# Kernel tuning notes

Measured on AMD Instinct MI355X. Metric: run time of the kernel, lower is better.

The kernel has to match this reference:

```python
import jax, jax.numpy as jnp
import numpy as np

N = 100000   # nodes
E = 1600000  # edges
D = 128      # input_dim == hidden_dim
G = 64       # graphs in batch
EPS = 1e-5


def setup_inputs() -> dict:
    key = jax.random.key(0)
    ks = jax.random.split(key, 16)
    s = 1.0 / np.sqrt(D)
    inp = {
        "x": jax.random.normal(ks[0], (N, D), jnp.float32),
        "edge_index": jax.random.randint(ks[1], (2, E), 0, N, jnp.int64),
        "batch": jnp.sort(jax.random.randint(ks[2], (N,), 0, G, jnp.int64)),
        # 4 blocks x 2 SAGEConv layers = 8 convs, all DxD
        "Wl": jax.random.normal(ks[3], (8, D, D), jnp.float32) * s,
        "bl": jnp.zeros((8, D), jnp.float32),
        "Wr": jax.random.normal(ks[4], (8, D, D), jnp.float32) * s,
        "gamma": jnp.ones((4, D), jnp.float32),
        "beta": jnp.zeros((4, D), jnp.float32),
        # classifier: 2D -> D -> D//2 -> 1
        "W1": jax.random.normal(ks[5], (2 * D, D), jnp.float32) / np.sqrt(2 * D),
        "b1": jnp.zeros((D,), jnp.float32),
        "W2": jax.random.normal(ks[6], (D, D // 2), jnp.float32) * s,
        "b2": jnp.zeros((D // 2,), jnp.float32),
        "W3": jax.random.normal(ks[7], (D // 2, 1), jnp.float32) / np.sqrt(D // 2),
        "b3": jnp.zeros((1,), jnp.float32),
    }
    return inp


def _sage_conv(h, src, dst, inv_deg, W_l, b_l, W_r):
    # mean-aggregate neighbor features (messages flow src -> dst)
    agg = jax.ops.segment_sum(h[src], dst, num_segments=N) * inv_deg
    return agg @ W_l + b_l + h @ W_r


def _forward(x, edge_index, batch, Wl, bl, Wr, gamma, beta, W1, b1, W2, b2, W3, b3):
    src, dst = edge_index[0], edge_index[1]
    deg = jax.ops.segment_sum(jnp.ones((E,), x.dtype), dst, num_segments=N)
    inv_deg = (1.0 / jnp.maximum(deg, 1.0))[:, None]  # [N,1]

    h = x
    for blk in range(4):
        # GraphSAGE(in, hid, num_layers=2): conv -> relu -> conv
        h = _sage_conv(h, src, dst, inv_deg, Wl[2 * blk], bl[2 * blk], Wr[2 * blk])
        h = jax.nn.relu(h)
        h = _sage_conv(h, src, dst, inv_deg, Wl[2 * blk + 1], bl[2 * blk + 1], Wr[2 * blk + 1])
        # BatchNorm1d over nodes (training-mode batch statistics, biased var)
        mu = jnp.mean(h, axis=0)
        var = jnp.var(h, axis=0)
        h = (h - mu) * jax.lax.rsqrt(var + EPS) * gamma[blk] + beta[blk]
        h = jax.nn.relu(h)  # dropout is identity in eval mode

    # global mean / max pool over graph ids
    cnt = jax.ops.segment_sum(jnp.ones((N,), h.dtype), batch, num_segments=G)
    x_mean = jax.ops.segment_sum(h, batch, num_segments=G) / jnp.maximum(cnt, 1.0)[:, None]
    x_max = jax.ops.segment_max(h, batch, num_segments=G)
    g = jnp.concatenate([x_mean, x_max], axis=1)  # [G, 2D]

    g = jax.nn.relu(g @ W1 + b1)
    g = jax.nn.relu(g @ W2 + b2)
    return g @ W3 + b3  # [G, 1]


def reference(x, edge_index, batch, Wl, bl, Wr, gamma, beta, W1, b1, W2, b2, W3, b3):
    return _forward(x, edge_index, batch, Wl, bl, Wr, gamma, beta, W1, b1, W2, b2, W3, b3)
```

## Files before the change

### kernel.cpp

```cpp
#include <hip/hip_runtime.h>
#include <hip/hip_bf16.h>
#include <math.h>

#define NN 100000
#define NE 1600000
#define DIM 128
#define NG 64
#define EPSBN 1e-5f
#define NGB 1563
#define SORT_WIN 12500
#define NBINBLK 6250
#define DSL 64

typedef unsigned int u32;
typedef unsigned short u16;
typedef __attribute__((ext_vector_type(8))) short bf8_t;
typedef __attribute__((ext_vector_type(4))) float f4_t;
typedef __attribute__((ext_vector_type(4))) unsigned short u16x4;
#define MFMA(a, b, c) __builtin_amdgcn_mfma_f32_16x16x32_bf16((a), (b), (c), 0, 0, 0)

__device__ __forceinline__ u16 f2bf(float f) {
    u32 u = __float_as_uint(f);
    u32 r = u + 0x7FFFu + ((u >> 16) & 1u);
    return (u16)(r >> 16);
}
__device__ __forceinline__ float bf2f(u16 h) { return __uint_as_float(((u32)h) << 16); }

__global__ void k_bin_cnt(const int* __restrict__ ei, int* __restrict__ blkcnt) {
    __shared__ int c[8];
    int t = threadIdx.x;
    if (t < 8) c[t] = 0;
    __syncthreads();
    int e = blockIdx.x * 256 + t;
    int d = ei[NE + e];
    atomicAdd(&c[d / SORT_WIN], 1);
    __syncthreads();
    if (t < 8) blkcnt[blockIdx.x * 8 + t] = c[t];
}

__global__ void k_bin_scan(const int* __restrict__ blkcnt, int* __restrict__ blkoff,
                           int* __restrict__ wtotal) {
    __shared__ int ps[256];
    int w = blockIdx.x, t = threadIdx.x;
    const int PER = (NBINBLK + 255) / 256;
    int s = 0;
    for (int i = 0; i < PER; ++i) {
        int b = t * PER + i;
        if (b < NBINBLK) s += blkcnt[b * 8 + w];
    }
    ps[t] = s;
    for (int off = 1; off < 256; off <<= 1) {
        __syncthreads();
        int x = (t >= off) ? ps[t - off] : 0;
        __syncthreads();
        ps[t] += x;
    }
    __syncthreads();
    int run = (t ? ps[t - 1] : 0);
    for (int i = 0; i < PER; ++i) {
        int b = t * PER + i;
        if (b < NBINBLK) { blkoff[b * 8 + w] = run; run += blkcnt[b * 8 + w]; }
    }
    if (t == 255) wtotal[w] = ps[255];
}

__global__ void k_bin_start(const int* __restrict__ wtotal, int* __restrict__ binStart) {
    if (threadIdx.x == 0) {
        int a = 0;
        for (int w = 0; w < 8; ++w) { binStart[w] = a; a += wtotal[w]; }
        binStart[8] = a;
    }
}

__global__ void k_bin_place(const int* __restrict__ ei, const int* __restrict__ blkoff,
                            const int* __restrict__ binStart, int2* __restrict__ binned) {
    __shared__ int base[8];
    int t = threadIdx.x;
    if (t < 8) base[t] = binStart[t] + blkoff[blockIdx.x * 8 + t];
    __syncthreads();
    int e = blockIdx.x * 256 + t;
    int s = ei[e], d = ei[NE + e];
    int pos = atomicAdd(&base[d / SORT_WIN], 1);
    binned[pos] = make_int2(s, d);
}

__global__ void k_deg2(const int2* __restrict__ binned, const int* __restrict__ binStart,
                       int* __restrict__ deg) {
    int w = blockIdx.x & 7, sl = blockIdx.x >> 3;
    int b0 = binStart[w], b1 = binStart[w + 1];
    int chunk = (b1 - b0 + DSL - 1) / DSL;
    int r0 = b0 + sl * chunk, r1 = min(r0 + chunk, b1);
    for (int i = r0 + threadIdx.x; i < r1; i += 256)
        atomicAdd(&deg[binned[i].y], 1);
}

__global__ void k_scatter(const int2* __restrict__ binned, const int* __restrict__ binStart,
                          int* __restrict__ cursor, int* __restrict__ sorted_src) {
    int w = blockIdx.x & 7, sl = blockIdx.x >> 3;
    int b0 = binStart[w], b1 = binStart[w + 1];
    int chunk = (b1 - b0 + DSL - 1) / DSL;
    int r0 = b0 + sl * chunk, r1 = min(r0 + chunk, b1);
    for (int i = r0 + threadIdx.x; i < r1; i += 256) {
        int2 e = binned[i];
        int pos = atomicAdd(&cursor[e.y], 1);
        sorted_src[pos] = e.x;
    }
}

#define SCAN_B 256
__global__ void k_scan1(const int* __restrict__ deg, int* __restrict__ row_start,
                        int* __restrict__ bsum, float* __restrict__ inv_deg) {
    __shared__ int s[SCAN_B];
    int t = threadIdx.x;
    int i = blockIdx.x * SCAN_B + t;
    int v = (i < NN) ? deg[i] : 0;
    if (i < NN) inv_deg[i] = 1.0f / (float)(v > 1 ? v : 1);
    s[t] = v;
    for (int off = 1; off < SCAN_B; off <<= 1) {
        __syncthreads();
        int x = (t >= off) ? s[t - off] : 0;
        __syncthreads();
        s[t] += x;
    }
    if (i < NN) row_start[i + 1] = s[t];
    if (t == SCAN_B - 1) bsum[blockIdx.x] = s[t];
}

__global__ void k_scan2(int* __restrict__ bsum, int nb) {
    __shared__ int s[512];
    int t = threadIdx.x;
    int v = (t < nb) ? bsum[t] : 0;
    s[t] = v;
    for (int off = 1; off < 512; off <<= 1) {
        __syncthreads();
        int x = (t >= off) ? s[t - off] : 0;
        __syncthreads();
        s[t] += x;
    }
    if (t < nb) bsum[t] = s[t] - v;
}

__global__ void k_scan3(int* __restrict__ row_start, const int* __restrict__ bsum,
                        int* __restrict__ cursor) {
    int i = blockIdx.x * blockDim.x + threadIdx.x;
    if (i < NN) {
        int v = row_start[i + 1] + bsum[i / SCAN_B];
        row_start[i + 1] = v;
        if (i + 1 < NN) cursor[i + 1] = v;
    }
    if (i == 0) { row_start[0] = 0; cursor[0] = 0; }
}

__global__ void k_bounds(const int* __restrict__ batch, int* __restrict__ gs) {
    int g = threadIdx.x;
    if (g > NG) return;
    int lo = 0, hi = NN;
    while (lo < hi) {
        int mid = (lo + hi) >> 1;
        if (batch[mid] < g) lo = mid + 1; else hi = mid;
    }
    gs[g] = lo;
}

__global__ void k_split_x(const float* __restrict__ x, u16* __restrict__ Xh,
                          u16* __restrict__ Xl) {
    int idx = blockIdx.x * 256 + threadIdx.x;
    int base = idx * 4;
    float4 v = *reinterpret_cast<const float4*>(&x[base]);
    u16x4 hi, lo;
    float vv[4] = {v.x, v.y, v.z, v.w};
#pragma unroll
    for (int j = 0; j < 4; j++) {
        u16 h = f2bf(vv[j]);
        hi[j] = h;
        lo[j] = f2bf(vv[j] - bf2f(h));
    }
    *reinterpret_cast<u16x4*>(&Xh[base]) = hi;
    *reinterpret_cast<u16x4*>(&Xl[base]) = lo;
}

__global__ void k_prep_w(const float* __restrict__ Wl, const float* __restrict__ Wr,
                         u16* __restrict__ Wth, u16* __restrict__ Wtl) {
    int idx = blockIdx.x * 256 + threadIdx.x;
    int k = idx & 255;
    int col = (idx >> 8) & 127;
    int c = idx >> 15;
    float v = (k < 128) ? Wl[(c * 128 + k) * 128 + col] : Wr[(c * 128 + (k - 128)) * 128 + col];
    u16 h = f2bf(v);
    Wth[idx] = h;
    Wtl[idx] = f2bf(v - bf2f(h));
}

template <int AFF>
__global__ void k_aggregate(const u16* __restrict__ Hh,
                            const int* __restrict__ row_start, const int* __restrict__ ssrc,
                            const float* __restrict__ inv_deg, const float* __restrict__ ss,
                            u16* __restrict__ Ah, u16* __restrict__ Al) {
    int wid = blockIdx.x * 4 + (threadIdx.x >> 6);
    int lane = threadIdx.x & 63;
    int half = lane >> 5;
    int cl = lane & 31;
    if (wid >= NN) return;
    float sc0 = 0.f, sc1 = 0.f, sc2 = 0.f, sc3 = 0.f;
    float sh0 = 0.f, sh1 = 0.f, sh2 = 0.f, sh3 = 0.f;
    if (AFF) {
        float4 s4 = *reinterpret_cast<const float4*>(ss + cl * 4);
        float4 h4 = *reinterpret_cast<const float4*>(ss + 128 + cl * 4);
        sc0 = s4.x; sc1 = s4.y; sc2 = s4.z; sc3 = s4.w;
        sh0 = h4.x; sh1 = h4.y; sh2 = h4.z; sh3 = h4.w;
    }
    int beg = row_start[wid], end = row_start[wid + 1];
    int n = end - beg;
    float a0 = 0.f, a1 = 0.f, a2 = 0.f, a3 = 0.f;
#define ACCUM(vv)                                                                   \
    {                                                                               \
        float t0 = __uint_as_float((vv).x << 16);                                   \
        float t1 = __uint_as_float((vv).x & 0xFFFF0000u);                           \
        float t2 = __uint_as_float((vv).y << 16);                                   \
        float t3 = __uint_as_float((vv).y & 0xFFFF0000u);                           \
        if (AFF) {                                                                  \
            t0 = fmaxf(t0 * sc0 + sh0, 0.f); t1 = fmaxf(t1 * sc1 + sh1, 0.f);       \
            t2 = fmaxf(t2 * sc2 + sh2, 0.f); t3 = fmaxf(t3 * sc3 + sh3, 0.f);       \
        }                                                                           \
        a0 += t0; a1 += t1; a2 += t2; a3 += t3;                                     \
    }
    for (int base = 0; base < n; base += 64) {
        int rem = n - base;
        int idx = beg + base + (lane < rem ? lane : 0);
        int sv = ssrc[idx];
        int m = rem < 64 ? rem : 64;
        int j = 0;
        for (; j + 4 <= m; j += 4) {
            int sA = __shfl(sv, j + half);
            int sB = __shfl(sv, j + 2 + half);
            uint2 vA = *reinterpret_cast<const uint2*>(
                reinterpret_cast<const u32*>(Hh + (size_t)sA * DIM) + cl * 2);
            uint2 vB = *reinterpret_cast<const uint2*>(
                reinterpret_cast<const u32*>(Hh + (size_t)sB * DIM) + cl * 2);
            ACCUM(vA); ACCUM(vB);
        }
        for (; j < m; j += 2) {
            if (j + half < m) {
                int s0 = __shfl(sv, j + half);
                uint2 v = *reinterpret_cast<const uint2*>(
                    reinterpret_cast<const u32*>(Hh + (size_t)s0 * DIM) + cl * 2);
                ACCUM(v);
            }
        }
    }
#undef ACCUM
    a0 += __shfl_down(a0, 32);
    a1 += __shfl_down(a1, 32);
    a2 += __shfl_down(a2, 32);
    a3 += __shfl_down(a3, 32);
    if (half == 0) {
        float sc = inv_deg[wid];
        a0 *= sc; a1 *= sc; a2 *= sc; a3 *= sc;
        u16 h0 = f2bf(a0), h1 = f2bf(a1), h2 = f2bf(a2), h3 = f2bf(a3);
        u16 l0 = f2bf(a0 - bf2f(h0)), l1 = f2bf(a1 - bf2f(h1));
        u16 l2 = f2bf(a2 - bf2f(h2)), l3 = f2bf(a3 - bf2f(h3));
        uint2 hv = make_uint2((u32)h0 | ((u32)h1 << 16), (u32)h2 | ((u32)h3 << 16));
        uint2 lv = make_uint2((u32)l0 | ((u32)l1 << 16), (u32)l2 | ((u32)l3 << 16));
        *reinterpret_cast<uint2*>(Ah + (size_t)wid * DIM + cl * 4) = hv;
        *reinterpret_cast<uint2*>(Al + (size_t)wid * DIM + cl * 4) = lv;
    }
}

__device__ __forceinline__ void affine_split(bf8_t& h, bf8_t& l,
                                             const float* __restrict__ ss, int k0) {
#pragma unroll
    for (int j = 0; j < 8; ++j) {
        float v = bf2f((u16)h[j]) + bf2f((u16)l[j]);
        v = fmaxf(v * ss[k0 + j] + ss[128 + k0 + j], 0.f);
        u16 hh = f2bf(v);
        h[j] = (short)hh;
        l[j] = (short)f2bf(v - bf2f(hh));
    }
}

template <bool RELU, bool STATS, bool AFF2>
__global__ __launch_bounds__(256, 2) void k_gemm(
    const u16* __restrict__ A1h, const u16* __restrict__ A1l,
    const u16* __restrict__ A2h, const u16* __restrict__ A2l,
    const u16* __restrict__ Wth, const u16* __restrict__ Wtl,
    const float* __restrict__ bias, const float* __restrict__ ss,
    u16* __restrict__ Oh, u16* __restrict__ Ol,
    float* __restrict__ partials) {
    __shared__ u16 sA[4][64][128];
    __shared__ float cs[128], cq[128];
    int t = threadIdx.x;
    int w = t >> 6, l = t & 63;
    int rl = l & 15, kg = l >> 4;
    int col0 = w * 32;
    int rbase = blockIdx.x * 64;

    const u16* srcs[4] = {A1h, A1l, A2h, A2l};
#pragma unroll
    for (int R = 0; R < 4; ++R) {
#pragma unroll
        for (int i = 0; i < 4; ++i) {
            int slot = i * 256 + w * 64 + l;
            int row = slot >> 4, cm = slot & 15;
            int cd = cm ^ (row & 7);
            int rowc = min(rbase + row, NN - 1);
            const u16* g = srcs[R] + (size_t)rowc * DIM + cd * 8;
            u16* lp = &sA[R][0][0] + (size_t)(i * 256 + w * 64) * 8;
            __builtin_amdgcn_global_load_lds(
                (const __attribute__((address_space(1))) void*)g,
                (__attribute__((address_space(3))) void*)lp, 16, 0, 0);
        }
    }
    asm volatile("s_waitcnt vmcnt(0)" ::: "memory");
    __syncthreads();

    f4_t acc[4][2];
#pragma unroll
    for (int i = 0; i < 4; ++i)
#pragma unroll
        for (int j = 0; j < 2; ++j) acc[i][j] = (f4_t){0.f, 0.f, 0.f, 0.f};

#define AFRAG(R, kc, rf)                                                            \
    (*reinterpret_cast<const bf8_t*>(                                               \
        &sA[(R)][(rf) * 16 + rl][((((kc) & 3) * 4 + kg) ^ (rl & 7)) * 8]))

#pragma unroll
    for (int kc = 0; kc < 8; ++kc) {
        int Rh = (kc < 4) ? 0 : 2;
        bf8_t wh0 = *reinterpret_cast<const bf8_t*>(
            Wth + (size_t)(col0 + rl) * 256 + kc * 32 + kg * 8);
        bf8_t wl0 = *reinterpret_cast<const bf8_t*>(
            Wtl + (size_t)(col0 + rl) * 256 + kc * 32 + kg * 8);
        bf8_t wh1 = *reinterpret_cast<const bf8_t*>(
            Wth + (size_t)(col0 + 16 + rl) * 256 + kc * 32 + kg * 8);
        bf8_t wl1 = *reinterpret_cast<const bf8_t*>(
            Wtl + (size_t)(col0 + 16 + rl) * 256 + kc * 32 + kg * 8);
#pragma unroll
        for (int rf = 0; rf < 4; ++rf) {
            bf8_t aH = AFRAG(Rh, kc, rf);
            bf8_t aL = AFRAG(Rh + 1, kc, rf);
            if (AFF2 && kc >= 4) {
                int k0 = (kc - 4) * 32 + kg * 8;
                affine_split(aH, aL, ss, k0);
            }
            acc[rf][0] = MFMA(aH, wh0, acc[rf][0]);
            acc[rf][0] = MFMA(aH, wl0, acc[rf][0]);
            acc[rf][0] = MFMA(aL, wh0, acc[rf][0]);
            acc[rf][1] = MFMA(aH, wh1, acc[rf][1]);
            acc[rf][1] = MFMA(aH, wl1, acc[rf][1]);
            acc[rf][1] = MFMA(aL, wh1, acc[rf][1]);
        }
    }
#undef AFRAG

    float bv0 = bias[col0 + rl];
    float bv1 = bias[col0 + 16 + rl];
    float s0 = 0.f, q0 = 0.f, s1 = 0.f, q1 = 0.f;
#pragma unroll
    for (int rf = 0; rf < 4; ++rf) {
#pragma unroll
        for (int i = 0; i < 4; ++i) {
            int row = rbase + rf * 16 + kg * 4 + i;
            if (row < NN) {
                float v = acc[rf][0][i] + bv0;
                if (RELU) v = fmaxf(v, 0.f);
                u16 hi = f2bf(v);
                Oh[(size_t)row * DIM + col0 + rl] = hi;
                Ol[(size_t)row * DIM + col0 + rl] = f2bf(v - bf2f(hi));
                if (STATS) { s0 += v; q0 += v * v; }
                float v1 = acc[rf][1][i] + bv1;
                if (RELU) v1 = fmaxf(v1, 0.f);
                u16 hi1 = f2bf(v1);
                Oh[(size_t)row * DIM + col0 + 16 + rl] = hi1;
                Ol[(size_t)row * DIM + col0 + 16 + rl] = f2bf(v1 - bf2f(hi1));
                if (STATS) { s1 += v1; q1 += v1 * v1; }
            }
        }
    }
    if (STATS) {
        s0 += __shfl_xor(s0, 16); s0 += __shfl_xor(s0, 32);
        q0 += __shfl_xor(q0, 16); q0 += __shfl_xor(q0, 32);
        s1 += __shfl_xor(s1, 16); s1 += __shfl_xor(s1, 32);
        q1 += __shfl_xor(q1, 16); q1 += __shfl_xor(q1, 32);
        if (l < 16) {
            cs[col0 + rl] = s0; cq[col0 + rl] = q0;
            cs[col0 + 16 + rl] = s1; cq[col0 + 16 + rl] = q1;
        }
        __syncthreads();
        partials[(size_t)blockIdx.x * 256 + t] = (t < 128) ? cs[t] : cq[t - 128];
    }
}

__global__ void k_bn_r1(const float* __restrict__ partials, float* __restrict__ colpart) {
    int t = threadIdx.x;
    int b = blockIdx.x;
    int b0 = b * 49, b1 = min(b0 + 49, NGB);
    float s = 0.f;
    for (int i = b0; i < b1; ++i) s += partials[i * 256 + t];
    colpart[b * 256 + t] = s;
}

__global__ void k_bn_r2(const float* __restrict__ colpart, const float* __restrict__ gamma,
                        const float* __restrict__ beta, float* __restrict__ scaleshift) {
    __shared__ float sm[256];
    int t = threadIdx.x;
    float s = 0.f;
#pragma unroll
    for (int b = 0; b < 32; ++b) s += colpart[b * 256 + t];
    sm[t] = s;
    __syncthreads();
    if (t < 128) {
        float mu = sm[t] * (1.0f / NN);
        float var = sm[t + 128] * (1.0f / NN) - mu * mu;
        float sc = rsqrtf(var + EPSBN) * gamma[t];
        scaleshift[t] = sc;
        scaleshift[t + 128] = beta[t] - mu * sc;
    }
}

__global__ void k_pool(const u16* __restrict__ Hh, const int* __restrict__ gs,
                       const float* __restrict__ ss,
                       float* __restrict__ pSum, float* __restrict__ pMax) {
    int g = blockIdx.x >> 3, slice = blockIdx.x & 7;
    int s0 = gs[g], s1 = gs[g + 1];
    int len = s1 - s0;
    int chunk = (len + 7) >> 3;
    int r0 = s0 + slice * chunk;
    int r1 = min(r0 + chunk, s1);
    int t = threadIdx.x;
    int c2 = (t & 63) * 2, half = t >> 6;
    float sc0 = ss[c2], sc1 = ss[c2 + 1];
    float sh0 = ss[128 + c2], sh1 = ss[128 + c2 + 1];
    float sa = 0.f, sb = 0.f, ma = 0.f, mb = 0.f;
    for (int r = r0 + half; r < r1; r += 4) {
        u32 h2 = *reinterpret_cast<const u32*>(Hh + r * DIM + c2);
        float v0 = fmaxf(__uint_as_float(h2 << 16) * sc0 + sh0, 0.f);
        float v1 = fmaxf(__uint_as_float(h2 & 0xFFFF0000u) * sc1 + sh1, 0.f);
        sa += v0; sb += v1;
        ma = fmaxf(ma, v0); mb = fmaxf(mb, v1);
    }
    __shared__ float ls[4][128], lm[4][128];
    ls[half][c2] = sa; ls[half][c2 + 1] = sb;
    lm[half][c2] = ma; lm[half][c2 + 1] = mb;
    __syncthreads();
    if (t < 128) {
        float s = ls[0][t] + ls[1][t] + ls[2][t] + ls[3][t];
        float m = fmaxf(fmaxf(lm[0][t], lm[1][t]), fmaxf(lm[2][t], lm[3][t]));
        atomicAdd(&pSum[g * DIM + t], s);
        atomicMax((int*)&pMax[g * DIM + t], __float_as_int(m));
    }
}

__global__ void k_mlp(const float* __restrict__ pSum, const float* __restrict__ pMax,
                      const int* __restrict__ gs,
                      const float* __restrict__ W1, const float* __restrict__ b1,
                      const float* __restrict__ W2, const float* __restrict__ b2,
                      const float* __restrict__ W3, const float* __restrict__ b3,
                      float* __restrict__ out) {
    __shared__ float g[256], y1[128], y2[64];
    int gi = blockIdx.x;
    int t = threadIdx.x;
    int cnt = gs[gi + 1] - gs[gi];
    float inv = 1.0f / fmaxf((float)cnt, 1.0f);
    g[t] = pSum[gi * DIM + t] * inv;
    g[128 + t] = pMax[gi * DIM + t];
    __syncthreads();
    float a = b1[t];
    for (int k = 0; k < 256; k++) a += g[k] * W1[k * 128 + t];
    y1[t] = fmaxf(a, 0.f);
    __syncthreads();
    if (t < 64) {
        float a2 = b2[t];
        for (int k = 0; k < 128; k++) a2 += y1[k] * W2[k * 64 + t];
        y2[t] = fmaxf(a2, 0.f);
    }
    __syncthreads();
    if (t < 64) {
        float p = y2[t] * W3[t];
#pragma unroll
        for (int off = 32; off; off >>= 1) p += __shfl_down(p, off);
        if (t == 0) out[gi] = p + b3[0];
    }
}

extern "C" void kernel_launch(void* const* d_in, const int* in_sizes, int n_in,
                              void* d_out, int out_size, void* d_ws, size_t ws_size,
                              hipStream_t stream) {
    const float* x     = (const float*)d_in[0];
    const int*   ei    = (const int*)d_in[1];
    const int*   batch = (const int*)d_in[2];
    const float* Wl    = (const float*)d_in[3];
    const float* bl    = (const float*)d_in[4];
    const float* Wr    = (const float*)d_in[5];
    const float* gamma = (const float*)d_in[6];
    const float* beta  = (const float*)d_in[7];
    const float* W1    = (const float*)d_in[8];
    const float* b1    = (const float*)d_in[9];
    const float* W2    = (const float*)d_in[10];
    const float* b2    = (const float*)d_in[11];
    const float* W3    = (const float*)d_in[12];
    const float* b3    = (const float*)d_in[13];
    float* out = (float*)d_out;

    char* p = (char*)d_ws;
    size_t off = 0;
    auto alloc = [&](size_t bytes) -> void* {
        void* r = p + off;
        off += (bytes + 255) & ~(size_t)255;
        return r;
    };
    const size_t HB = (size_t)NN * DIM * 2;
    u16* Xh   = (u16*)alloc(HB);
    u16* Xl   = (u16*)alloc(HB);
    u16* hAh  = (u16*)alloc(HB);
    u16* hAl  = (u16*)alloc(HB);
    u16* aggh = (u16*)alloc(HB);
    u16* aggl = (u16*)alloc(HB);
    int*   ssrc      = (int*)alloc((size_t)NE * 4);
    u16*   Wth       = (u16*)alloc((size_t)8 * 128 * 256 * 2);
    u16*   Wtl       = (u16*)alloc((size_t)8 * 128 * 256 * 2);
    float* partials  = (float*)alloc((size_t)NGB * 256 * 4);
    float* colpart   = (float*)alloc(32 * 256 * 4);
    int*   deg       = (int*)alloc(NN * 4);
    float* inv_deg   = (float*)alloc(NN * 4);
    int*   row_start = (int*)alloc((NN + 1) * 4);
    int*   cursor    = (int*)alloc(NN * 4);
    int*   bsum      = (int*)alloc(512 * 4);
    int*   gs        = (int*)alloc((NG + 1) * 4);
    int*   blkcnt    = (int*)alloc((size_t)NBINBLK * 8 * 4);
    int*   blkoff    = (int*)alloc((size_t)NBINBLK * 8 * 4);
    int*   wtotal    = (int*)alloc(8 * 4);
    int*   binStart  = (int*)alloc(9 * 4);
    float* ssb       = (float*)alloc(4 * 256 * 4);
    float* pSum      = (float*)alloc(NG * DIM * 4);
    float* pMax      = (float*)alloc(NG * DIM * 4);
    int2*  binned    = (int2*)aggh;

    const int nbN = (NN + 255) / 256;
    const int nbQ = NN * DIM / 4 / 256;
    const int aggGrid = (NN + 3) / 4;

    hipMemsetAsync(deg, 0, NN * 4, stream);
    k_bin_cnt<<<NBINBLK, 256, 0, stream>>>(ei, blkcnt);
    k_bin_scan<<<8, 256, 0, stream>>>(blkcnt, blkoff, wtotal);
    k_bin_start<<<1, 64, 0, stream>>>(wtotal, binStart);
    k_bin_place<<<NBINBLK, 256, 0, stream>>>(ei, blkoff, binStart, binned);
    k_deg2<<<8 * DSL, 256, 0, stream>>>(binned, binStart, deg);
    k_scan1<<<nbN, 256, 0, stream>>>(deg, row_start, bsum, inv_deg);
    k_scan2<<<1, 512, 0, stream>>>(bsum, nbN);
    k_scan3<<<nbN, 256, 0, stream>>>(row_start, bsum, cursor);
    k_scatter<<<8 * DSL, 256, 0, stream>>>(binned, binStart, cursor, ssrc);
    k_bounds<<<1, 128, 0, stream>>>(batch, gs);

    k_split_x<<<nbQ, 256, 0, stream>>>(x, Xh, Xl);
    k_prep_w<<<8 * 128 * 256 / 256, 256, 0, stream>>>(Wl, Wr, Wth, Wtl);

    for (int b = 0; b < 4; b++) {
        int c0 = 2 * b, c1 = 2 * b + 1;
        const u16* W0h = Wth + (size_t)c0 * 128 * 256;
        const u16* W0l = Wtl + (size_t)c0 * 128 * 256;
        const u16* W1h = Wth + (size_t)c1 * 128 * 256;
        const u16* W1l = Wtl + (size_t)c1 * 128 * 256;
        const float* ssPrev = ssb + (size_t)(b > 0 ? b - 1 : 0) * 256;
        if (b == 0) {
            k_aggregate<0><<<aggGrid, 256, 0, stream>>>(Xh, row_start, ssrc, inv_deg,
                                                        ssPrev, aggh, aggl);
            k_gemm<true, false, false><<<NGB, 256, 0, stream>>>(
                aggh, aggl, Xh, Xl, W0h, W0l, bl + c0 * DIM, ssPrev, hAh, hAl, partials);
        } else {
            k_aggregate<1><<<aggGrid, 256, 0, stream>>>(Xh, row_start, ssrc, inv_deg,
                                                        ssPrev, aggh, aggl);
            k_gemm<true, false, true><<<NGB, 256, 0, stream>>>(
                aggh, aggl, Xh, Xl, W0h, W0l, bl + c0 * DIM, ssPrev, hAh, hAl, partials);
        }
        k_aggregate<0><<<aggGrid, 256, 0, stream>>>(hAh, row_start, ssrc, inv_deg,
                                                    ssPrev, aggh, aggl);
        k_gemm<false, true, false><<<NGB, 256, 0, stream>>>(
            aggh, aggl, hAh, hAl, W1h, W1l, bl + c1 * DIM, ssPrev, Xh, Xl, partials);
        k_bn_r1<<<32, 256, 0, stream>>>(partials, colpart);
        k_bn_r2<<<1, 256, 0, stream>>>(colpart, gamma + b * DIM, beta + b * DIM,
                                       ssb + (size_t)b * 256);
    }

    hipMemsetAsync(pSum, 0, NG * DIM * 4, stream);
    hipMemsetAsync(pMax, 0, NG * DIM * 4, stream);
    k_pool<<<NG * 8, 256, 0, stream>>>(Xh, gs, ssb + 3 * 256, pSum, pMax);
    k_mlp<<<NG, 128, 0, stream>>>(pSum, pMax, gs, W1, b1, W2, b2, W3, b3, out);
}
```

Measured before the change: 1.398 ms.

## Fuse neighbor aggregation into the SAGE GEMM kernel via shared memory

Merges the separate aggregate and GEMM kernels into one k_conv kernel. Each 512-thread block gathers the mean of neighbor features for its 64 rows straight into LDS as bf16, while async loads bring the self features into LDS, then runs the MFMA GEMM. This removes the global write and re-read of the split hi/lo aggregate buffers and half the launches. It also drops the low-order bf16 part of the aggregate (fewer MFMAs, less precision), and the per-block gather now runs on fewer waves per node tile, which may affect latency hiding.

```diff
diff --git a/kernel.cpp b/kernel.cpp
--- a/kernel.cpp
+++ b/kernel.cpp
@@ -191,202 +191,184 @@
     Wtl[idx] = f2bf(v - bf2f(h));
 }
 
-template <int AFF>
-__global__ void k_aggregate(const u16* __restrict__ Hh,
-                            const int* __restrict__ row_start, const int* __restrict__ ssrc,
-                            const float* __restrict__ inv_deg, const float* __restrict__ ss,
-                            u16* __restrict__ Ah, u16* __restrict__ Al) {
-    int wid = blockIdx.x * 4 + (threadIdx.x >> 6);
-    int lane = threadIdx.x & 63;
-    int half = lane >> 5;
-    int cl = lane & 31;
-    if (wid >= NN) return;
-    float sc0 = 0.f, sc1 = 0.f, sc2 = 0.f, sc3 = 0.f;
-    float sh0 = 0.f, sh1 = 0.f, sh2 = 0.f, sh3 = 0.f;
-    if (AFF) {
-        float4 s4 = *reinterpret_cast<const float4*>(ss + cl * 4);
-        float4 h4 = *reinterpret_cast<const float4*>(ss + 128 + cl * 4);
-        sc0 = s4.x; sc1 = s4.y; sc2 = s4.z; sc3 = s4.w;
-        sh0 = h4.x; sh1 = h4.y; sh2 = h4.z; sh3 = h4.w;
-    }
-    int beg = row_start[wid], end = row_start[wid + 1];
-    int n = end - beg;
-    float a0 = 0.f, a1 = 0.f, a2 = 0.f, a3 = 0.f;
+__device__ __forceinline__ void affine_split(bf8_t& h, bf8_t& l,
+                                             const float* __restrict__ ss, int k0) {
+#pragma unroll
+    for (int j = 0; j < 8; ++j) {
+        float v = bf2f((u16)h[j]) + bf2f((u16)l[j]);
+        v = fmaxf(v * ss[k0 + j] + ss[128 + k0 + j], 0.f);
+        u16 hh = f2bf(v);
+        h[j] = (short)hh;
+        l[j] = (short)f2bf(v - bf2f(hh));
+    }
+}
+
+template <bool AFFG, bool STATS, bool AFF2, bool RELU>
+__global__ __launch_bounds__(512, 6) void k_conv(
+    const u16* __restrict__ Ah, const u16* __restrict__ Al,
+    const int* __restrict__ row_start, const int* __restrict__ ssrc,
+    const float* __restrict__ inv_deg,
+    const u16* __restrict__ Wth, const u16* __restrict__ Wtl,
+    const float* __restrict__ bias, const float* __restrict__ ss,
+    u16* __restrict__ Oh, u16* __restrict__ Ol,
+    float* __restrict__ partials) {
+    __shared__ u16 sAgg[64][128];
+    __shared__ u16 sX[2][64][128];
+    __shared__ float cs[128], cq[128];
+    int t = threadIdx.x;
+    int w = t >> 6, l = t & 63;
+    int rbase = blockIdx.x * 64;
+
+#pragma unroll
+    for (int R = 0; R < 2; ++R) {
+        const u16* src = R ? Al : Ah;
+#pragma unroll
+        for (int i = 0; i < 2; ++i) {
+            int slot = i * 512 + t;
+            int row = slot >> 4, cm = slot & 15;
+            int cd = cm ^ (row & 7);
+            int rowc = min(rbase + row, NN - 1);
+            const u16* g = src + (size_t)rowc * DIM + cd * 8;
+            u16* lp = &sX[R][0][0] + (size_t)(i * 512 + w * 64) * 8;
+            __builtin_amdgcn_global_load_lds(
+                (const __attribute__((address_space(1))) void*)g,
+                (__attribute__((address_space(3))) void*)lp, 16, 0, 0);
+        }
+    }
+
+    {
+        int half = l >> 5;
+        int cl = l & 31;
+        float sc0 = 0.f, sc1 = 0.f, sc2 = 0.f, sc3 = 0.f;
+        float sh0 = 0.f, sh1 = 0.f, sh2 = 0.f, sh3 = 0.f;
+        if (AFFG) {
+            float4 s4 = *reinterpret_cast<const float4*>(ss + cl * 4);
+            float4 h4 = *reinterpret_cast<const float4*>(ss + 128 + cl * 4);
+            sc0 = s4.x; sc1 = s4.y; sc2 = s4.z; sc3 = s4.w;
+            sh0 = h4.x; sh1 = h4.y; sh2 = h4.z; sh3 = h4.w;
+        }
+        for (int q = 0; q < 8; ++q) {
+            int wid = rbase + w * 8 + q;
+            if (wid < NN) {
+                int beg = row_start[wid], end = row_start[wid + 1];
+                int n = end - beg;
+                float a0 = 0.f, a1 = 0.f, a2 = 0.f, a3 = 0.f;
 #define ACCUM(vv)                                                                   \
     {                                                                               \
         float t0 = __uint_as_float((vv).x << 16);                                   \
         float t1 = __uint_as_float((vv).x & 0xFFFF0000u);                           \
         float t2 = __uint_as_float((vv).y << 16);                                   \
         float t3 = __uint_as_float((vv).y & 0xFFFF0000u);                           \
-        if (AFF) {                                                                  \
+        if (AFFG) {                                                                 \
             t0 = fmaxf(t0 * sc0 + sh0, 0.f); t1 = fmaxf(t1 * sc1 + sh1, 0.f);       \
             t2 = fmaxf(t2 * sc2 + sh2, 0.f); t3 = fmaxf(t3 * sc3 + sh3, 0.f);       \
         }                                                                           \
         a0 += t0; a1 += t1; a2 += t2; a3 += t3;                                     \
     }
-    for (int base = 0; base < n; base += 64) {
-        int rem = n - base;
-        int idx = beg + base + (lane < rem ? lane : 0);
-        int sv = ssrc[idx];
-        int m = rem < 64 ? rem : 64;
-        int j = 0;
-        for (; j + 4 <= m; j += 4) {
-            int sA = __shfl(sv, j + half);
-            int sB = __shfl(sv, j + 2 + half);
-            uint2 vA = *reinterpret_cast<const uint2*>(
-                reinterpret_cast<const u32*>(Hh + (size_t)sA * DIM) + cl * 2);
-            uint2 vB = *reinterpret_cast<const uint2*>(
-                reinterpret_cast<const u32*>(Hh + (size_t)sB * DIM) + cl * 2);
-            ACCUM(vA); ACCUM(vB);
-        }
-        for (; j < m; j += 2) {
-            if (j + half < m) {
-                int s0 = __shfl(sv, j + half);
-                uint2 v = *reinterpret_cast<const uint2*>(
-                    reinterpret_cast<const u32*>(Hh + (size_t)s0 * DIM) + cl * 2);
-                ACCUM(v);
+                for (int base = 0; base < n; base += 64) {
+                    int rem = n - base;
+                    int idx = beg + base + (l < rem ? l : 0);
+                    int sv = ssrc[idx];
+                    int m = rem < 64 ? rem : 64;
+                    int j = 0;
+                    for (; j + 4 <= m; j += 4) {
+                        int sA = __shfl(sv, j + half);
+                        int sB = __shfl(sv, j + 2 + half);
+                        uint2 vA = *reinterpret_cast<const uint2*>(
+                            reinterpret_cast<const u32*>(Ah + (size_t)sA * DIM) + cl * 2);
+                        uint2 vB = *reinterpret_cast<const uint2*>(
+                            reinterpret_cast<const u32*>(Ah + (size_t)sB * DIM) + cl * 2);
+                        ACCUM(vA); ACCUM(vB);
+                    }
+                    for (; j < m; j += 2) {
+                        if (j + half < m) {
+                            int s0 = __shfl(sv, j + half);
+                            uint2 v = *reinterpret_cast<const uint2*>(
+                                reinterpret_cast<const u32*>(Ah + (size_t)s0 * DIM) + cl * 2);
+                            ACCUM(v);
+                        }
+                    }
+                }
+#undef ACCUM
+                a0 += __shfl_down(a0, 32);
+                a1 += __shfl_down(a1, 32);
+                a2 += __shfl_down(a2, 32);
+                a3 += __shfl_down(a3, 32);
+                if (half == 0) {
+                    float sc = inv_deg[wid];
+                    a0 *= sc; a1 *= sc; a2 *= sc; a3 *= sc;
+                    u32 p0 = (u32)f2bf(a0) | ((u32)f2bf(a1) << 16);
+                    u32 p1 = (u32)f2bf(a2) | ((u32)f2bf(a3) << 16);
+                    int row = w * 8 + q;
+                    u16* dst = &sAgg[row][(((cl >> 1) ^ (row & 7)) << 3) + ((cl & 1) << 2)];
+                    *reinterpret_cast<uint2*>(dst) = make_uint2(p0, p1);
+                }
             }
         }
     }
-#undef ACCUM
-    a0 += __shfl_down(a0, 32);
-    a1 += __shfl_down(a1, 32);
-    a2 += __shfl_down(a2, 32);
-    a3 += __shfl_down(a3, 32);
-    if (half == 0) {
-        float sc = inv_deg[wid];
-        a0 *= sc; a1 *= sc; a2 *= sc; a3 *= sc;
-        u16 h0 = f2bf(a0), h1 = f2bf(a1), h2 = f2bf(a2), h3 = f2bf(a3);
-        u16 l0 = f2bf(a0 - bf2f(h0)), l1 = f2bf(a1 - bf2f(h1));
-        u16 l2 = f2bf(a2 - bf2f(h2)), l3 = f2bf(a3 - bf2f(h3));
-        uint2 hv = make_uint2((u32)h0 | ((u32)h1 << 16), (u32)h2 | ((u32)h3 << 16));
-        uint2 lv = make_uint2((u32)l0 | ((u32)l1 << 16), (u32)l2 | ((u32)l3 << 16));
-        *reinterpret_cast<uint2*>(Ah + (size_t)wid * DIM + cl * 4) = hv;
-        *reinterpret_cast<uint2*>(Al + (size_t)wid * DIM + cl * 4) = lv;
-    }
-}
-
-__device__ __forceinline__ void affine_split(bf8_t& h, bf8_t& l,
-                                             const float* __restrict__ ss, int k0) {
-#pragma unroll
-    for (int j = 0; j < 8; ++j) {
-        float v = bf2f((u16)h[j]) + bf2f((u16)l[j]);
-        v = fmaxf(v * ss[k0 + j] + ss[128 + k0 + j], 0.f);
-        u16 hh = f2bf(v);
-        h[j] = (short)hh;
-        l[j] = (short)f2bf(v - bf2f(hh));
-    }
-}
-
-template <bool RELU, bool STATS, bool AFF2>
-__global__ __launch_bounds__(256, 2) void k_gemm(
-    const u16* __restrict__ A1h, const u16* __restrict__ A1l,
-    const u16* __restrict__ A2h, const u16* __restrict__ A2l,
-    const u16* __restrict__ Wth, const u16* __restrict__ Wtl,
-    const float* __restrict__ bias, const float* __restrict__ ss,
-    u16* __restrict__ Oh, u16* __restrict__ Ol,
-    float* __restrict__ partials) {
-    __shared__ u16 sA[4][64][128];
-    __shared__ float cs[128], cq[128];
-    int t = threadIdx.x;
-    int w = t >> 6, l = t & 63;
+    asm volatile("s_waitcnt vmcnt(0)" ::: "memory");
+    __syncthreads();
+
     int rl = l & 15, kg = l >> 4;
-    int col0 = w * 32;
-    int rbase = blockIdx.x * 64;
-
-    const u16* srcs[4] = {A1h, A1l, A2h, A2l};
-#pragma unroll
-    for (int R = 0; R < 4; ++R) {
-#pragma unroll
-        for (int i = 0; i < 4; ++i) {
-            int slot = i * 256 + w * 64 + l;
-            int row = slot >> 4, cm = slot & 15;
-            int cd = cm ^ (row & 7);
-            int rowc = min(rbase + row, NN - 1);
-            const u16* g = srcs[R] + (size_t)rowc * DIM + cd * 8;
-            u16* lp = &sA[R][0][0] + (size_t)(i * 256 + w * 64) * 8;
-            __builtin_amdgcn_global_load_lds(
-                (const __attribute__((address_space(1))) void*)g,
-                (__attribute__((address_space(3))) void*)lp, 16, 0, 0);
-        }
-    }
-    asm volatile("s_waitcnt vmcnt(0)" ::: "memory");
-    __syncthreads();
-
-    f4_t acc[4][2];
-#pragma unroll
-    for (int i = 0; i < 4; ++i)
-#pragma unroll
-        for (int j = 0; j < 2; ++j) acc[i][j] = (f4_t){0.f, 0.f, 0.f, 0.f};
-
-#define AFRAG(R, kc, rf)                                                            \
-    (*reinterpret_cast<const bf8_t*>(                                               \
-        &sA[(R)][(rf) * 16 + rl][((((kc) & 3) * 4 + kg) ^ (rl & 7)) * 8]))
+    int col0 = w * 16;
+    f4_t acc[4];
+#pragma unroll
+    for (int i = 0; i < 4; ++i) acc[i] = (f4_t){0.f, 0.f, 0.f, 0.f};
 
 #pragma unroll
     for (int kc = 0; kc < 8; ++kc) {
-        int Rh = (kc < 4) ? 0 : 2;
-        bf8_t wh0 = *reinterpret_cast<const bf8_t*>(
+        bf8_t wh = *reinterpret_cast<const bf8_t*>(
             Wth + (size_t)(col0 + rl) * 256 + kc * 32 + kg * 8);
-        bf8_t wl0 = *reinterpret_cast<const bf8_t*>(
+        bf8_t wl_ = *reinterpret_cast<const bf8_t*>(
             Wtl + (size_t)(col0 + rl) * 256 + kc * 32 + kg * 8);
-        bf8_t wh1 = *reinterpret_cast<const bf8_t*>(
-            Wth + (size_t)(col0 + 16 + rl) * 256 + kc * 32 + kg * 8);
-        bf8_t wl1 = *reinterpret_cast<const bf8_t*>(
-            Wtl + (size_t)(col0 + 16 + rl) * 256 + kc * 32 + kg * 8);
 #pragma unroll
         for (int rf = 0; rf < 4; ++rf) {
-            bf8_t aH = AFRAG(Rh, kc, rf);
-            bf8_t aL = AFRAG(Rh + 1, kc, rf);
-            if (AFF2 && kc >= 4) {
-                int k0 = (kc - 4) * 32 + kg * 8;
-                affine_split(aH, aL, ss, k0);
+            int row = rf * 16 + rl;
+            int cd = (((kc & 3) * 4 + kg) ^ (row & 7)) * 8;
+            if (kc < 4) {
+                bf8_t aH = *reinterpret_cast<const bf8_t*>(&sAgg[row][cd]);
+                acc[rf] = MFMA(aH, wh, acc[rf]);
+                acc[rf] = MFMA(aH, wl_, acc[rf]);
+            } else {
+                bf8_t aH = *reinterpret_cast<const bf8_t*>(&sX[0][row][cd]);
+                bf8_t aL = *reinterpret_cast<const bf8_t*>(&sX[1][row][cd]);
+                if (AFF2) {
+                    int k0 = (kc - 4) * 32 + kg * 8;
+                    affine_split(aH, aL, ss, k0);
+                }
+                acc[rf] = MFMA(aH, wh, acc[rf]);
+                acc[rf] = MFMA(aH, wl_, acc[rf]);
+                acc[rf] = MFMA(aL, wh, acc[rf]);
             }
-            acc[rf][0] = MFMA(aH, wh0, acc[rf][0]);
-            acc[rf][0] = MFMA(aH, wl0, acc[rf][0]);
-            acc[rf][0] = MFMA(aL, wh0, acc[rf][0]);
-            acc[rf][1] = MFMA(aH, wh1, acc[rf][1]);
-            acc[rf][1] = MFMA(aH, wl1, acc[rf][1]);
-            acc[rf][1] = MFMA(aL, wh1, acc[rf][1]);
-        }
-    }
-#undef AFRAG
-
-    float bv0 = bias[col0 + rl];
-    float bv1 = bias[col0 + 16 + rl];
-    float s0 = 0.f, q0 = 0.f, s1 = 0.f, q1 = 0.f;
+        }
+    }
+
+    float bv = bias[col0 + rl];
+    float s0 = 0.f, q0 = 0.f;
 #pragma unroll
     for (int rf = 0; rf < 4; ++rf) {
 #pragma unroll
         for (int i = 0; i < 4; ++i) {
             int row = rbase + rf * 16 + kg * 4 + i;
             if (row < NN) {
-                float v = acc[rf][0][i] + bv0;
+                float v = acc[rf][i] + bv;
                 if (RELU) v = fmaxf(v, 0.f);
                 u16 hi = f2bf(v);
                 Oh[(size_t)row * DIM + col0 + rl] = hi;
                 Ol[(size_t)row * DIM + col0 + rl] = f2bf(v - bf2f(hi));
                 if (STATS) { s0 += v; q0 += v * v; }
-                float v1 = acc[rf][1][i] + bv1;
-                if (RELU) v1 = fmaxf(v1, 0.f);
-                u16 hi1 = f2bf(v1);
-                Oh[(size_t)row * DIM + col0 + 16 + rl] = hi1;
-                Ol[(size_t)row * DIM + col0 + 16 + rl] = f2bf(v1 - bf2f(hi1));
-                if (STATS) { s1 += v1; q1 += v1 * v1; }
             }
         }
     }
     if (STATS) {
         s0 += __shfl_xor(s0, 16); s0 += __shfl_xor(s0, 32);
         q0 += __shfl_xor(q0, 16); q0 += __shfl_xor(q0, 32);
-        s1 += __shfl_xor(s1, 16); s1 += __shfl_xor(s1, 32);
-        q1 += __shfl_xor(q1, 16); q1 += __shfl_xor(q1, 32);
         if (l < 16) {
-            cs[col0 + rl] = s0; cq[col0 + rl] = q0;
-            cs[col0 + 16 + rl] = s1; cq[col0 + 16 + rl] = q1;
-        }
-        __syncthreads();
-        partials[(size_t)blockIdx.x * 256 + t] = (t < 128) ? cs[t] : cq[t - 128];
+            cs[col0 + rl] = s0;
+            cq[col0 + rl] = q0;
+        }
+        __syncthreads();
+        if (t < 256) partials[(size_t)blockIdx.x * 256 + t] = (t < 128) ? cs[t] : cq[t - 128];
     }
 }
 
@@ -513,8 +495,7 @@
     u16* Xl   = (u16*)alloc(HB);
     u16* hAh  = (u16*)alloc(HB);
     u16* hAl  = (u16*)alloc(HB);
-    u16* aggh = (u16*)alloc(HB);
-    u16* aggl = (u16*)alloc(HB);
+    int2*  binned    = (int2*)alloc((size_t)NE * 8);
     int*   ssrc      = (int*)alloc((size_t)NE * 4);
     u16*   Wth       = (u16*)alloc((size_t)8 * 128 * 256 * 2);
     u16*   Wtl       = (u16*)alloc((size_t)8 * 128 * 256 * 2);
@@ -533,11 +514,9 @@
     float* ssb       = (float*)alloc(4 * 256 * 4);
     float* pSum      = (float*)alloc(NG * DIM * 4);
     float* pMax      = (float*)alloc(NG * DIM * 4);
-    int2*  binned    = (int2*)aggh;
 
     const int nbN = (NN + 255) / 256;
     const int nbQ = NN * DIM / 4 / 256;
-    const int aggGrid = (NN + 3) / 4;
 
     hipMemsetAsync(deg, 0, NN * 4, stream);
     k_bin_cnt<<<NBINBLK, 256, 0, stream>>>(ei, blkcnt);
@@ -562,20 +541,17 @@
         const u16* W1l = Wtl + (size_t)c1 * 128 * 256;
         const float* ssPrev = ssb + (size_t)(b > 0 ? b - 1 : 0) * 256;
         if (b == 0) {
-            k_aggregate<0><<<aggGrid, 256, 0, stream>>>(Xh, row_start, ssrc, inv_deg,
-                                                        ssPrev, aggh, aggl);
-            k_gemm<true, false, false><<<NGB, 256, 0, stream>>>(
-                aggh, aggl, Xh, Xl, W0h, W0l, bl + c0 * DIM, ssPrev, hAh, hAl, partials);
+            k_conv<false, false, false, true><<<NGB, 512, 0, stream>>>(
+                Xh, Xl, row_start, ssrc, inv_deg, W0h, W0l, bl + c0 * DIM, ssPrev,
+                hAh, hAl, partials);
         } else {
-            k_aggregate<1><<<aggGrid, 256, 0, stream>>>(Xh, row_start, ssrc, inv_deg,
-                                                        ssPrev, aggh, aggl);
-            k_gemm<true, false, true><<<NGB, 256, 0, stream>>>(
-                aggh, aggl, Xh, Xl, W0h, W0l, bl + c0 * DIM, ssPrev, hAh, hAl, partials);
-        }
-        k_aggregate<0><<<aggGrid, 256, 0, stream>>>(hAh, row_start, ssrc, inv_deg,
-                                                    ssPrev, aggh, aggl);
-        k_gemm<false, true, false><<<NGB, 256, 0, stream>>>(
-            aggh, aggl, hAh, hAl, W1h, W1l, bl + c1 * DIM, ssPrev, Xh, Xl, partials);
+            k_conv<true, false, true, true><<<NGB, 512, 0, stream>>>(
+                Xh, Xl, row_start, ssrc, inv_deg, W0h, W0l, bl + c0 * DIM, ssPrev,
+                hAh, hAl, partials);
+        }
+        k_conv<false, true, false, false><<<NGB, 512, 0, stream>>>(
+            hAh, hAl, row_start, ssrc, inv_deg, W1h, W1l, bl + c1 * DIM, ssPrev,
+            Xh, Xl, partials);
         k_bn_r1<<<32, 256, 0, stream>>>(partials, colpart);
         k_bn_r2<<<1, 256, 0, stream>>>(colpart, gamma + b * DIM, beta + b * DIM,
                                        ssb + (size_t)b * 256);
```

New measurement: 1.428 ms. 2.1% more time.

## Halve GEMM row tile to raise occupancy and unroll gather by eight

Applied to the files above, without the earlier changes.

The split-bf16 GEMM kernel now processes 32 rows per block instead of 64. This halves LDS and accumulator use, and the launch bound is raised to four blocks per CU for better latency hiding. The boundary clamp is dropped because 100000 divides evenly by 32, and the BN partial reduction is resized for the doubled block count. The neighbor aggregation loop gains an 8-wide unrolled path so more independent gather loads are in flight. The cost is that each weight fragment is reused across fewer rows, which adds weight reloads and more partials to reduce.

```diff
diff --git a/kernel.cpp b/kernel.cpp
--- a/kernel.cpp
+++ b/kernel.cpp
@@ -7,7 +7,7 @@
 #define DIM 128
 #define NG 64
 #define EPSBN 1e-5f
-#define NGB 1563
+#define NGB 3125
 #define SORT_WIN 12500
 #define NBINBLK 6250
 #define DSL 64
@@ -230,6 +230,21 @@
         int sv = ssrc[idx];
         int m = rem < 64 ? rem : 64;
         int j = 0;
+        for (; j + 8 <= m; j += 8) {
+            int s0i = __shfl(sv, j + half);
+            int s1i = __shfl(sv, j + 2 + half);
+            int s2i = __shfl(sv, j + 4 + half);
+            int s3i = __shfl(sv, j + 6 + half);
+            uint2 v0 = *reinterpret_cast<const uint2*>(
+                reinterpret_cast<const u32*>(Hh + (size_t)s0i * DIM) + cl * 2);
+            uint2 v1 = *reinterpret_cast<const uint2*>(
+                reinterpret_cast<const u32*>(Hh + (size_t)s1i * DIM) + cl * 2);
+            uint2 v2 = *reinterpret_cast<const uint2*>(
+                reinterpret_cast<const u32*>(Hh + (size_t)s2i * DIM) + cl * 2);
+            uint2 v3 = *reinterpret_cast<const uint2*>(
+                reinterpret_cast<const u32*>(Hh + (size_t)s3i * DIM) + cl * 2);
+            ACCUM(v0); ACCUM(v1); ACCUM(v2); ACCUM(v3);
+        }
         for (; j + 4 <= m; j += 4) {
             int sA = __shfl(sv, j + half);
             int sB = __shfl(sv, j + 2 + half);
@@ -241,9 +256,9 @@
         }
         for (; j < m; j += 2) {
             if (j + half < m) {
-                int s0 = __shfl(sv, j + half);
+                int s0i = __shfl(sv, j + half);
                 uint2 v = *reinterpret_cast<const uint2*>(
-                    reinterpret_cast<const u32*>(Hh + (size_t)s0 * DIM) + cl * 2);
+                    reinterpret_cast<const u32*>(Hh + (size_t)s0i * DIM) + cl * 2);
                 ACCUM(v);
             }
         }
@@ -279,31 +294,30 @@
 }
 
 template <bool RELU, bool STATS, bool AFF2>
-__global__ __launch_bounds__(256, 2) void k_gemm(
+__global__ __launch_bounds__(256, 4) void k_gemm(
     const u16* __restrict__ A1h, const u16* __restrict__ A1l,
     const u16* __restrict__ A2h, const u16* __restrict__ A2l,
     const u16* __restrict__ Wth, const u16* __restrict__ Wtl,
     const float* __restrict__ bias, const float* __restrict__ ss,
     u16* __restrict__ Oh, u16* __restrict__ Ol,
     float* __restrict__ partials) {
-    __shared__ u16 sA[4][64][128];
+    __shared__ u16 sA[4][32][128];
     __shared__ float cs[128], cq[128];
     int t = threadIdx.x;
     int w = t >> 6, l = t & 63;
     int rl = l & 15, kg = l >> 4;
     int col0 = w * 32;
-    int rbase = blockIdx.x * 64;
+    int rbase = blockIdx.x * 32;
 
     const u16* srcs[4] = {A1h, A1l, A2h, A2l};
 #pragma unroll
     for (int R = 0; R < 4; ++R) {
 #pragma unroll
-        for (int i = 0; i < 4; ++i) {
-            int slot = i * 256 + w * 64 + l;
+        for (int i = 0; i < 2; ++i) {
+            int slot = i * 256 + t;
             int row = slot >> 4, cm = slot & 15;
             int cd = cm ^ (row & 7);
-            int rowc = min(rbase + row, NN - 1);
-            const u16* g = srcs[R] + (size_t)rowc * DIM + cd * 8;
+            const u16* g = srcs[R] + (size_t)(rbase + row) * DIM + cd * 8;
             u16* lp = &sA[R][0][0] + (size_t)(i * 256 + w * 64) * 8;
             __builtin_amdgcn_global_load_lds(
                 (const __attribute__((address_space(1))) void*)g,
@@ -313,15 +327,11 @@
     asm volatile("s_waitcnt vmcnt(0)" ::: "memory");
     __syncthreads();
 
-    f4_t acc[4][2];
-#pragma unroll
-    for (int i = 0; i < 4; ++i)
+    f4_t acc[2][2];
+#pragma unroll
+    for (int i = 0; i < 2; ++i)
 #pragma unroll
         for (int j = 0; j < 2; ++j) acc[i][j] = (f4_t){0.f, 0.f, 0.f, 0.f};
-
-#define AFRAG(R, kc, rf)                                                            \
-    (*reinterpret_cast<const bf8_t*>(                                               \
-        &sA[(R)][(rf) * 16 + rl][((((kc) & 3) * 4 + kg) ^ (rl & 7)) * 8]))
 
 #pragma unroll
     for (int kc = 0; kc < 8; ++kc) {
@@ -335,9 +345,11 @@
         bf8_t wl1 = *reinterpret_cast<const bf8_t*>(
             Wtl + (size_t)(col0 + 16 + rl) * 256 + kc * 32 + kg * 8);
 #pragma unroll
-        for (int rf = 0; rf < 4; ++rf) {
-            bf8_t aH = AFRAG(Rh, kc, rf);
-            bf8_t aL = AFRAG(Rh + 1, kc, rf);
+        for (int rf = 0; rf < 2; ++rf) {
+            int row = rf * 16 + rl;
+            int cd = (((kc & 3) * 4 + kg) ^ (row & 7)) * 8;
+            bf8_t aH = *reinterpret_cast<const bf8_t*>(&sA[Rh][row][cd]);
+            bf8_t aL = *reinterpret_cast<const bf8_t*>(&sA[Rh + 1][row][cd]);
             if (AFF2 && kc >= 4) {
                 int k0 = (kc - 4) * 32 + kg * 8;
                 affine_split(aH, aL, ss, k0);
@@ -350,30 +362,27 @@
             acc[rf][1] = MFMA(aL, wh1, acc[rf][1]);
         }
     }
-#undef AFRAG
 
     float bv0 = bias[col0 + rl];
     float bv1 = bias[col0 + 16 + rl];
     float s0 = 0.f, q0 = 0.f, s1 = 0.f, q1 = 0.f;
 #pragma unroll
-    for (int rf = 0; rf < 4; ++rf) {
+    for (int rf = 0; rf < 2; ++rf) {
 #pragma unroll
         for (int i = 0; i < 4; ++i) {
             int row = rbase + rf * 16 + kg * 4 + i;
-            if (row < NN) {
-                float v = acc[rf][0][i] + bv0;
-                if (RELU) v = fmaxf(v, 0.f);
-                u16 hi = f2bf(v);
-                Oh[(size_t)row * DIM + col0 + rl] = hi;
-                Ol[(size_t)row * DIM + col0 + rl] = f2bf(v - bf2f(hi));
-                if (STATS) { s0 += v; q0 += v * v; }
-                float v1 = acc[rf][1][i] + bv1;
-                if (RELU) v1 = fmaxf(v1, 0.f);
-                u16 hi1 = f2bf(v1);
-                Oh[(size_t)row * DIM + col0 + 16 + rl] = hi1;
-                Ol[(size_t)row * DIM + col0 + 16 + rl] = f2bf(v1 - bf2f(hi1));
-                if (STATS) { s1 += v1; q1 += v1 * v1; }
-            }
+            float v = acc[rf][0][i] + bv0;
+            if (RELU) v = fmaxf(v, 0.f);
+            u16 hi = f2bf(v);
+            Oh[(size_t)row * DIM + col0 + rl] = hi;
+            Ol[(size_t)row * DIM + col0 + rl] = f2bf(v - bf2f(hi));
+            if (STATS) { s0 += v; q0 += v * v; }
+            float v1 = acc[rf][1][i] + bv1;
+            if (RELU) v1 = fmaxf(v1, 0.f);
+            u16 hi1 = f2bf(v1);
+            Oh[(size_t)row * DIM + col0 + 16 + rl] = hi1;
+            Ol[(size_t)row * DIM + col0 + 16 + rl] = f2bf(v1 - bf2f(hi1));
+            if (STATS) { s1 += v1; q1 += v1 * v1; }
         }
     }
     if (STATS) {
@@ -393,7 +402,7 @@
 __global__ void k_bn_r1(const float* __restrict__ partials, float* __restrict__ colpart) {
     int t = threadIdx.x;
     int b = blockIdx.x;
-    int b0 = b * 49, b1 = min(b0 + 49, NGB);
+    int b0 = b * 98, b1 = min(b0 + 98, NGB);
     float s = 0.f;
     for (int i = b0; i < b1; ++i) s += partials[i * 256 + t];
     colpart[b * 256 + t] = s;
```

Result: slower. 1.445 ms (+3.4%).
